# Kernel tuning notes

Measured on AMD Instinct MI355X. Metric: run time of the kernel, lower is better.

Reference implementation:

```python
import jax, jax.numpy as jnp
import numpy as np

B, NF, QUERY_DIM = 4, 300, 512
HIDDEN, NUM_HEADS = 512, 8
H, W = 80, 80
HEAD_DIM = HIDDEN // NUM_HEADS
NORM_FACT = float(HIDDEN / NUM_HEADS) ** (-0.5)


def setup_inputs() -> dict:
    key = jax.random.key(0)
    k1, k2, k3, k4, k5 = jax.random.split(key, 5)
    # xavier_uniform bound for [HIDDEN, QUERY_DIM] weight
    bound = float(np.sqrt(6.0 / (HIDDEN + QUERY_DIM)))
    return {
        "q": jax.random.normal(k1, (B, NF, QUERY_DIM), dtype=jnp.float32),
        "k": jax.random.normal(k2, (B, QUERY_DIM, H, W), dtype=jnp.float32),
        "mask": jax.random.bernoulli(k3, 0.25, (B, H, W)),  # True = masked out
        "q_w": jax.random.uniform(k4, (HIDDEN, QUERY_DIM), jnp.float32, -bound, bound),
        "q_b": jnp.zeros((HIDDEN,), jnp.float32),
        "k_w": jax.random.uniform(k5, (HIDDEN, QUERY_DIM), jnp.float32, -bound, bound),
        "k_b": jnp.zeros((HIDDEN,), jnp.float32),
    }


def reference(q, k, mask, q_w, q_b, k_w, k_b):
    b, nf, _ = q.shape
    h, w = k.shape[-2], k.shape[-1]
    # q projection: [b, nf, hidden]
    qp = jnp.einsum("bqd,ed->bqe", q, q_w) + q_b
    # k projection (1x1 conv == channel matmul): [b, hidden, h, w]
    kp = jnp.einsum("bdhw,ed->behw", k, k_w) + k_b[None, :, None, None]
    # split heads
    qh = qp.reshape(b, nf, NUM_HEADS, HEAD_DIM) * NORM_FACT   # [b,q,n,c]
    kh = kp.reshape(b, NUM_HEADS, HEAD_DIM, h, w)             # [b,n,c,h,w]
    # batched QK scores (replaces the per-query python loop + cat(dim=2))
    weights = jnp.einsum("bqnc,bnchw->bqnhw", qh, kh)
    weights = weights.reshape(b, 1, nf * NUM_HEADS, h, w)
    # masked_fill with -inf on padded spatial positions
    weights = jnp.where(mask[:, None, None, :, :], -jnp.inf, weights)
    # NOTE: softmax over flatten(2) = jointly over (queries*heads*h*w), as in source
    weights = jax.nn.softmax(weights.reshape(b, 1, -1), axis=-1)
    return weights.reshape(b, 1, nf * NUM_HEADS, h, w)
```

## Files before the change

### kernel.cpp

```cpp
#include <hip/hip_runtime.h>
#include <math.h>

#define B_    4
#define NF    300
#define QD    512
#define HID   512
#define NH    8
#define HD    64
#define HW    6400
#define ROWS  2400
#define NQP   384
#define NORM_FACT 0.125f
#define NEG_INF (-INFINITY)
#define LDK   40

typedef __bf16 bf16_t;
typedef __bf16 bf16x4_t __attribute__((ext_vector_type(4)));
typedef __bf16 bf16x8_t __attribute__((ext_vector_type(8)));
typedef float  f32x4    __attribute__((ext_vector_type(4)));

__device__ __forceinline__ void splitf(float x, bf16_t& h, bf16_t& l) {
    h = (bf16_t)x;
    l = (bf16_t)(x - (float)h);
}
__device__ __forceinline__ int swz(int c, int row) {
    return (((c >> 3) ^ (row & 7)) << 3) | (c & 7);
}

__device__ __forceinline__ void qproj_body(
    char* smem, int blk, const float* __restrict__ q,
    const float* __restrict__ qw, const float* __restrict__ qb,
    bf16_t* __restrict__ qh_hi, bf16_t* __restrict__ qh_lo)
{
    float (*qs)[QD] = (float (*)[QD])smem;
    const int r0    = blk * 4;
    const int b     = r0 / NF;
    const int qbase = r0 % NF;
    const int t     = threadIdx.x;
    #pragma unroll
    for (int row = 0; row < 4; ++row) {
        qs[row][t]       = q[(size_t)(r0 + row) * QD + t];
        qs[row][t + 256] = q[(size_t)(r0 + row) * QD + t + 256];
    }
    __syncthreads();
    #pragma unroll
    for (int eo = 0; eo < 2; ++eo) {
        const int e = t + eo * 256;
        const int n = e >> 6, c = e & 63;
        float a[4] = {0.f, 0.f, 0.f, 0.f};
        for (int d = 0; d < QD; d += 4) {
            float4 w = *(const float4*)&qw[(size_t)e * QD + d];
            #pragma unroll
            for (int row = 0; row < 4; ++row)
                a[row] += qs[row][d]*w.x + qs[row][d+1]*w.y
                        + qs[row][d+2]*w.z + qs[row][d+3]*w.w;
        }
        const float bias = qb[e];
        #pragma unroll
        for (int row = 0; row < 4; ++row) {
            const int qq = qbase + row;
            const float val = (a[row] + bias) * NORM_FACT;
            bf16_t h, l; splitf(val, h, l);
            size_t off = ((size_t)(b * NH + n) * NQP + qq) * 64 + swz(c, qq);
            qh_hi[off] = h; qh_lo[off] = l;
        }
    }
}

__device__ __forceinline__ void kproj_body(
    char* smem, int px, int ey, int b, const float* __restrict__ k,
    const float* __restrict__ kw, const float* __restrict__ kb,
    bf16_t* __restrict__ kp_hi, bf16_t* __restrict__ kp_lo)
{
    bf16_t (*Ah)[LDK] = (bf16_t (*)[LDK])(smem);
    bf16_t (*Al)[LDK] = (bf16_t (*)[LDK])(smem + 10240);
    bf16_t (*Bh)[LDK] = (bf16_t (*)[LDK])(smem + 20480);
    bf16_t (*Bl)[LDK] = (bf16_t (*)[LDK])(smem + 30720);
    const int e0 = ey * 128;
    const int p0 = px * 128;
    const int t  = threadIdx.x;
    const int wave = t >> 6, lane = t & 63;
    const int wr = wave >> 1, wc = wave & 1;
    const int lm = lane & 15, lq = lane >> 4;
    const float* kB = k + (size_t)b * QD * HW;

    f32x4 acc[4][4];
    const f32x4 zero4 = {0.f, 0.f, 0.f, 0.f};
    #pragma unroll
    for (int i = 0; i < 4; ++i)
        #pragma unroll
        for (int j = 0; j < 4; ++j) acc[i][j] = zero4;

    for (int d0 = 0; d0 < QD; d0 += 32) {
        #pragma unroll
        for (int i = 0; i < 4; ++i) {
            int idx = t + i * 256;
            int p = idx & 127, db = (idx >> 7) << 2;
            bf16x4_t hv, lv;
            #pragma unroll
            for (int j = 0; j < 4; ++j) {
                float x = kB[(size_t)(d0 + db + j) * HW + p0 + p];
                bf16_t hx, lx; splitf(x, hx, lx);
                hv[j] = hx; lv[j] = lx;
            }
            *(bf16x4_t*)&Ah[p][db] = hv;
            *(bf16x4_t*)&Al[p][db] = lv;
        }
        #pragma unroll
        for (int i = 0; i < 4; ++i) {
            int idx = t + i * 256;
            int e = idx >> 3, dp = (idx & 7) << 2;
            float4 v = *(const float4*)&kw[(size_t)(e0 + e) * QD + d0 + dp];
            bf16x4_t hv, lv; bf16_t hx, lx;
            splitf(v.x, hx, lx); hv[0] = hx; lv[0] = lx;
            splitf(v.y, hx, lx); hv[1] = hx; lv[1] = lx;
            splitf(v.z, hx, lx); hv[2] = hx; lv[2] = lx;
            splitf(v.w, hx, lx); hv[3] = hx; lv[3] = lx;
            *(bf16x4_t*)&Bh[e][dp] = hv;
            *(bf16x4_t*)&Bl[e][dp] = lv;
        }
        __syncthreads();

        bf16x8_t ah[4], al[4], bh[4], bl[4];
        #pragma unroll
        for (int mt = 0; mt < 4; ++mt) {
            int r = wr * 64 + mt * 16 + lm;
            ah[mt] = *(const bf16x8_t*)&Ah[r][lq * 8];
            al[mt] = *(const bf16x8_t*)&Al[r][lq * 8];
        }
        #pragma unroll
        for (int nt = 0; nt < 4; ++nt) {
            int c = wc * 64 + nt * 16 + lm;
            bh[nt] = *(const bf16x8_t*)&Bh[c][lq * 8];
            bl[nt] = *(const bf16x8_t*)&Bl[c][lq * 8];
        }
        #pragma unroll
        for (int mt = 0; mt < 4; ++mt)
            #pragma unroll
            for (int nt = 0; nt < 4; ++nt) {
                f32x4 a = acc[mt][nt];
                a = __builtin_amdgcn_mfma_f32_16x16x32_bf16(al[mt], bh[nt], a, 0, 0, 0);
                a = __builtin_amdgcn_mfma_f32_16x16x32_bf16(ah[mt], bl[nt], a, 0, 0, 0);
                a = __builtin_amdgcn_mfma_f32_16x16x32_bf16(ah[mt], bh[nt], a, 0, 0, 0);
                acc[mt][nt] = a;
            }
        __syncthreads();
    }

    #pragma unroll
    for (int nt = 0; nt < 4; ++nt) {
        const int e = e0 + wc * 64 + nt * 16 + lm;
        const int n = e >> 6;
        const int c = (nt * 16 + lm) & 63;
        const float bias = kb[e];
        bf16_t* dh = kp_hi + (size_t)(b * NH + n) * HW * 64;
        bf16_t* dl = kp_lo + (size_t)(b * NH + n) * HW * 64;
        #pragma unroll
        for (int mt = 0; mt < 4; ++mt) {
            #pragma unroll
            for (int reg = 0; reg < 4; ++reg) {
                int p = p0 + wr * 64 + mt * 16 + lq * 4 + reg;
                float val = acc[mt][nt][reg] + bias;
                bf16_t h, l; splitf(val, h, l);
                size_t off = (size_t)p * 64 + swz(c, p);
                dh[off] = h; dl[off] = l;
            }
        }
    }
}

__global__ __launch_bounds__(256) void proj_kernel(
    const float* __restrict__ q, const float* __restrict__ qw,
    const float* __restrict__ qb, const float* __restrict__ k,
    const float* __restrict__ kw, const float* __restrict__ kb,
    bf16_t* __restrict__ qh_hi, bf16_t* __restrict__ qh_lo,
    bf16_t* __restrict__ kp_hi, bf16_t* __restrict__ kp_lo)
{
    __shared__ __align__(16) char smem[40960];
    const int bx = blockIdx.x;
    if (bx < 800) {
        kproj_body(smem, bx % 50, (bx / 50) % 4, bx / 200, k, kw, kb, kp_hi, kp_lo);
    } else {
        qproj_body(smem, bx - 800, q, qw, qb, qh_hi, qh_lo);
    }
}

template<int KS>
__device__ __forceinline__ void load_qf(const bf16_t* __restrict__ qp,
                                        int lm, int lq, bf16x8_t (&f)[4])
{
    #pragma unroll
    for (int nt = 0; nt < 4; ++nt) {
        const size_t o = (size_t)(nt * 16 + lm) * 64
                       + (size_t)((((KS * 4 + lq) ^ (lm & 7))) << 3);
        f[nt] = *(const bf16x8_t*)(qp + o);
    }
}

template<int KS>
__device__ __forceinline__ void ks_mfma_hi(const bf16_t* Kh, int wr, int lm, int lq,
                                           const bf16x8_t (&qh)[4], f32x4 (&acc)[4][4])
{
    #pragma unroll
    for (int mt = 0; mt < 4; ++mt) {
        const int row = wr * 64 + mt * 16 + lm;
        const int off = row * 64 + ((((KS * 4 + lq) ^ (lm & 7))) << 3);
        const bf16x8_t ah = *(const bf16x8_t*)&Kh[off];
        #pragma unroll
        for (int nt = 0; nt < 4; ++nt)
            acc[mt][nt] = __builtin_amdgcn_mfma_f32_16x16x32_bf16(
                ah, qh[nt], acc[mt][nt], 0, 0, 0);
    }
}

template<int KS>
__device__ __forceinline__ void ks_mfma_split(const bf16_t* Kh, const bf16_t* Kl,
                                              int wr, int lm, int lq,
                                              const bf16x8_t (&qh)[4],
                                              const bf16x8_t (&ql)[4],
                                              f32x4 (&acc)[4][4])
{
    #pragma unroll
    for (int mt = 0; mt < 4; ++mt) {
        const int row = wr * 64 + mt * 16 + lm;
        const int off = row * 64 + ((((KS * 4 + lq) ^ (lm & 7))) << 3);
        const bf16x8_t ah = *(const bf16x8_t*)&Kh[off];
        const bf16x8_t al = *(const bf16x8_t*)&Kl[off];
        #pragma unroll
        for (int nt = 0; nt < 4; ++nt) {
            f32x4 a = acc[mt][nt];
            a = __builtin_amdgcn_mfma_f32_16x16x32_bf16(al, qh[nt], a, 0, 0, 0);
            a = __builtin_amdgcn_mfma_f32_16x16x32_bf16(ah, ql[nt], a, 0, 0, 0);
            a = __builtin_amdgcn_mfma_f32_16x16x32_bf16(ah, qh[nt], a, 0, 0, 0);
            acc[mt][nt] = a;
        }
    }
}

__global__ __launch_bounds__(256, 4) void scores_pass_a(
    const bf16_t* __restrict__ qh_hi, const bf16_t* __restrict__ kp_hi,
    const int* __restrict__ mask, float* __restrict__ partials)
{
    __shared__ __align__(16) bf16_t Kh[128 * 64];
    __shared__ float redM[256];
    __shared__ float redS[256];
    const int z  = blockIdx.z;
    const int b  = z >> 3, n = z & 7;
    const int q0 = blockIdx.y * 128;
    const int p0 = blockIdx.x * 128;
    const int t  = threadIdx.x;
    const int wave = t >> 6, lane = t & 63;
    const int wr = wave >> 1, wc = wave & 1;
    const int lm = lane & 15, lq = lane >> 4;
    const bool wave_active = (q0 + wc * 64) < NF;

    const uint4* gb = (const uint4*)(kp_hi + ((size_t)(b * NH + n) * HW + p0) * 64);
    uint4* lb = (uint4*)Kh;
    #pragma unroll
    for (int i = 0; i < 4; ++i) lb[t + i * 256] = gb[t + i * 256];

    const bf16_t* qph = qh_hi + ((size_t)(b * NH + n) * NQP + q0 + wc * 64) * 64;
    bf16x8_t qf0[4];
    if (wave_active) load_qf<0>(qph, lm, lq, qf0);
    __syncthreads();

    float tm = NEG_INF, ts = 0.f;
    if (wave_active) {
        f32x4 acc[4][4];
        const f32x4 zero4 = {0.f, 0.f, 0.f, 0.f};
        #pragma unroll
        for (int i = 0; i < 4; ++i)
            #pragma unroll
            for (int j = 0; j < 4; ++j) acc[i][j] = zero4;

        bf16x8_t qf1[4];
        load_qf<1>(qph, lm, lq, qf1);
        ks_mfma_hi<0>(Kh, wr, lm, lq, qf0, acc);
        ks_mfma_hi<1>(Kh, wr, lm, lq, qf1, acc);

        int4 mm4[4];
        #pragma unroll
        for (int mt = 0; mt < 4; ++mt)
            mm4[mt] = *(const int4*)&mask[b * HW + p0 + wr * 64 + mt * 16 + lq * 4];

        #pragma unroll
        for (int nt = 0; nt < 4; ++nt) {
            if (q0 + wc * 64 + nt * 16 + lm < NF) {
                #pragma unroll
                for (int mt = 0; mt < 4; ++mt)
                    #pragma unroll
                    for (int reg = 0; reg < 4; ++reg)
                        if (!((const int*)&mm4[mt])[reg])
                            tm = fmaxf(tm, acc[mt][nt][reg]);
            }
        }
        if (tm != NEG_INF) {
            #pragma unroll
            for (int nt = 0; nt < 4; ++nt) {
                if (q0 + wc * 64 + nt * 16 + lm < NF) {
                    #pragma unroll
                    for (int mt = 0; mt < 4; ++mt)
                        #pragma unroll
                        for (int reg = 0; reg < 4; ++reg)
                            if (!((const int*)&mm4[mt])[reg])
                                ts += __expf(acc[mt][nt][reg] - tm);
                }
            }
        }
    }

    redM[t] = tm; redS[t] = ts;
    __syncthreads();
    for (int off = 128; off > 0; off >>= 1) {
        if (t < off) {
            float m1 = redM[t],       s1 = redS[t];
            float m2 = redM[t + off], s2 = redS[t + off];
            float M = fmaxf(m1, m2);
            float s = (M == NEG_INF) ? 0.f
                      : (s1 * __expf(m1 - M) + s2 * __expf(m2 - M));
            redM[t] = M; redS[t] = s;
        }
        __syncthreads();
    }
    if (t == 0) {
        int lin = (z * gridDim.y + blockIdx.y) * gridDim.x + blockIdx.x;
        partials[2 * lin]     = redM[0];
        partials[2 * lin + 1] = redS[0];
    }
}

__global__ __launch_bounds__(256) void stats_kernel(
    const float* __restrict__ partials, float* __restrict__ stats, int nper)
{
    __shared__ float redM[256];
    __shared__ float redS[256];
    const int b = blockIdx.x, t = threadIdx.x;
    const float* p = partials + (size_t)b * nper * 2;
    float m = NEG_INF, s = 0.f;
    for (int i = t; i < nper; i += 256) {
        float m2 = p[2 * i], s2 = p[2 * i + 1];
        float M = fmaxf(m, m2);
        float ns = (M == NEG_INF) ? 0.f
                   : (s * __expf(m - M) + s2 * __expf(m2 - M));
        m = M; s = ns;
    }
    redM[t] = m; redS[t] = s;
    __syncthreads();
    for (int off = 128; off > 0; off >>= 1) {
        if (t < off) {
            float m1 = redM[t],       s1 = redS[t];
            float m2 = redM[t + off], s2 = redS[t + off];
            float M = fmaxf(m1, m2);
            float ns = (M == NEG_INF) ? 0.f
                       : (s1 * __expf(m1 - M) + s2 * __expf(m2 - M));
            redM[t] = M; redS[t] = ns;
        }
        __syncthreads();
    }
    if (t == 0) {
        stats[2 * b]     = redM[0];
        stats[2 * b + 1] = 1.0f / redS[0];
    }
}

__global__ __launch_bounds__(256, 3) void scores_pass_b(
    const bf16_t* __restrict__ qh_hi, const bf16_t* __restrict__ qh_lo,
    const bf16_t* __restrict__ kp_hi, const bf16_t* __restrict__ kp_lo,
    const int* __restrict__ mask, const float* __restrict__ stats,
    float* __restrict__ out)
{
    __shared__ __align__(16) bf16_t Kh[128 * 64];
    __shared__ __align__(16) bf16_t Kl[128 * 64];
    const int z  = blockIdx.z;
    const int b  = z >> 3, n = z & 7;
    const int q0 = blockIdx.y * 128;
    const int p0 = blockIdx.x * 128;
    const int t  = threadIdx.x;
    const int wave = t >> 6, lane = t & 63;
    const int wr = wave >> 1, wc = wave & 1;
    const int lm = lane & 15, lq = lane >> 4;
    const bool wave_active = (q0 + wc * 64) < NF;

    const float M    = stats[2 * b];
    const float invS = stats[2 * b + 1];

    const size_t bbase = ((size_t)(b * NH + n) * HW + p0) * 64;
    const uint4* gbh = (const uint4*)(kp_hi + bbase);
    const uint4* gbl = (const uint4*)(kp_lo + bbase);
    #pragma unroll
    for (int i = 0; i < 4; ++i) {
        ((uint4*)Kh)[t + i * 256] = gbh[t + i * 256];
        ((uint4*)Kl)[t + i * 256] = gbl[t + i * 256];
    }

    const size_t qoff = ((size_t)(b * NH + n) * NQP + q0 + wc * 64) * 64;
    const bf16_t* qph = qh_hi + qoff;
    const bf16_t* qpl = qh_lo + qoff;
    bf16x8_t qh0[4], ql0[4];
    if (wave_active) {
        load_qf<0>(qph, lm, lq, qh0);
        load_qf<0>(qpl, lm, lq, ql0);
    }
    __syncthreads();
    if (!wave_active) return;

    f32x4 acc[4][4];
    const f32x4 zero4 = {0.f, 0.f, 0.f, 0.f};
    #pragma unroll
    for (int i = 0; i < 4; ++i)
        #pragma unroll
        for (int j = 0; j < 4; ++j) acc[i][j] = zero4;

    bf16x8_t qh1[4], ql1[4];
    load_qf<1>(qph, lm, lq, qh1);
    load_qf<1>(qpl, lm, lq, ql1);
    ks_mfma_split<0>(Kh, Kl, wr, lm, lq, qh0, ql0, acc);
    ks_mfma_split<1>(Kh, Kl, wr, lm, lq, qh1, ql1, acc);

    int4 mm4[4];
    #pragma unroll
    for (int mt = 0; mt < 4; ++mt)
        mm4[mt] = *(const int4*)&mask[b * HW + p0 + wr * 64 + mt * 16 + lq * 4];

    #pragma unroll
    for (int nt = 0; nt < 4; ++nt) {
        const int qg = q0 + wc * 64 + nt * 16 + lm;
        if (qg < NF) {
            float* rowp = out + (size_t)(b * ROWS + qg * NH + n) * HW + p0 + wr * 64;
            #pragma unroll
            for (int mt = 0; mt < 4; ++mt) {
                f32x4 v;
                #pragma unroll
                for (int reg = 0; reg < 4; ++reg) {
                    const int msk = ((const int*)&mm4[mt])[reg];
                    v[reg] = msk ? 0.f : __expf(acc[mt][nt][reg] - M) * invS;
                }
                __builtin_nontemporal_store(v, (f32x4*)(rowp + mt * 16 + lq * 4));
            }
        }
    }
}

extern "C" void kernel_launch(void* const* d_in, const int* in_sizes, int n_in,
                              void* d_out, int out_size, void* d_ws, size_t ws_size,
                              hipStream_t stream) {
    const float* q    = (const float*)d_in[0];
    const float* k    = (const float*)d_in[1];
    const int*   mask = (const int*)  d_in[2];
    const float* qw   = (const float*)d_in[3];
    const float* qb   = (const float*)d_in[4];
    const float* kw   = (const float*)d_in[5];
    const float* kb   = (const float*)d_in[6];
    float* out = (float*)d_out;

    bf16_t* kp_hi = (bf16_t*)d_ws;
    bf16_t* kp_lo = kp_hi + (size_t)B_ * NH * HW * 64;
    bf16_t* qh_hi = kp_lo + (size_t)B_ * NH * HW * 64;
    bf16_t* qh_lo = qh_hi + (size_t)B_ * NH * NQP * 64;
    float* partials = (float*)(qh_lo + (size_t)B_ * NH * NQP * 64);
    float* stats    = partials + 2 * 4800;

    proj_kernel<<<1100, 256, 0, stream>>>(q, qw, qb, k, kw, kb,
                                          qh_hi, qh_lo, kp_hi, kp_lo);
    scores_pass_a<<<dim3(50, 3, 32), 256, 0, stream>>>(qh_hi, kp_hi, mask, partials);
    stats_kernel<<<4, 256, 0, stream>>>(partials, stats, 1200);
    scores_pass_b<<<dim3(50, 3, 32), 256, 0, stream>>>(qh_hi, qh_lo, kp_hi, kp_lo,
                                                       mask, stats, out);
}
```

Baseline: 477.0 us.

## Pre-split K and weights to bf16 hi/lo, use direct global-to-LDS loads

```diff
diff --git a/kernel.cpp b/kernel.cpp
--- a/kernel.cpp
+++ b/kernel.cpp
@@ -12,12 +12,11 @@
 #define NQP   384
 #define NORM_FACT 0.125f
 #define NEG_INF (-INFINITY)
-#define LDK   40
 
 typedef __bf16 bf16_t;
-typedef __bf16 bf16x4_t __attribute__((ext_vector_type(4)));
 typedef __bf16 bf16x8_t __attribute__((ext_vector_type(8)));
 typedef float  f32x4    __attribute__((ext_vector_type(4)));
+typedef unsigned int u32;
 
 __device__ __forceinline__ void splitf(float x, bf16_t& h, bf16_t& l) {
     h = (bf16_t)x;
@@ -26,63 +25,127 @@
 __device__ __forceinline__ int swz(int c, int row) {
     return (((c >> 3) ^ (row & 7)) << 3) | (c & 7);
 }
-
-__device__ __forceinline__ void qproj_body(
-    char* smem, int blk, const float* __restrict__ q,
-    const float* __restrict__ qw, const float* __restrict__ qb,
+__device__ __forceinline__ void gload_lds16(const bf16_t* g, bf16_t* l) {
+    __builtin_amdgcn_global_load_lds(
+        (const __attribute__((address_space(1))) u32*)g,
+        (__attribute__((address_space(3))) u32*)l, 16, 0, 0);
+}
+
+__global__ __launch_bounds__(256) void presplit_kernel(
+    const float* __restrict__ k, const float* __restrict__ kw,
+    const float* __restrict__ q, const float* __restrict__ qw,
+    const float* __restrict__ qb,
+    bf16_t* __restrict__ kt_hi, bf16_t* __restrict__ kt_lo,
+    bf16_t* __restrict__ wh, bf16_t* __restrict__ wl,
     bf16_t* __restrict__ qh_hi, bf16_t* __restrict__ qh_lo)
 {
-    float (*qs)[QD] = (float (*)[QD])smem;
-    const int r0    = blk * 4;
-    const int b     = r0 / NF;
-    const int qbase = r0 % NF;
-    const int t     = threadIdx.x;
-    #pragma unroll
-    for (int row = 0; row < 4; ++row) {
-        qs[row][t]       = q[(size_t)(r0 + row) * QD + t];
-        qs[row][t + 256] = q[(size_t)(r0 + row) * QD + t + 256];
-    }
-    __syncthreads();
-    #pragma unroll
-    for (int eo = 0; eo < 2; ++eo) {
-        const int e = t + eo * 256;
-        const int n = e >> 6, c = e & 63;
-        float a[4] = {0.f, 0.f, 0.f, 0.f};
-        for (int d = 0; d < QD; d += 4) {
-            float4 w = *(const float4*)&qw[(size_t)e * QD + d];
-            #pragma unroll
-            for (int row = 0; row < 4; ++row)
-                a[row] += qs[row][d]*w.x + qs[row][d+1]*w.y
-                        + qs[row][d+2]*w.z + qs[row][d+3]*w.w;
-        }
-        const float bias = qb[e];
+    __shared__ __align__(16) char smem[64 * 65 * 4];
+    const int blk = blockIdx.x;
+    const int t   = threadIdx.x;
+
+    if (blk < 3200) {
+        float (*ts)[65] = (float (*)[65])smem;
+        const int b   = blk / 800;
+        const int rem = blk % 800;
+        const int d0  = (rem / 100) * 64;
+        const int p0  = (rem % 100) * 64;
+        const float* kB = k + (size_t)b * QD * HW;
+        const int c = t & 63, r0 = t >> 6;
+        #pragma unroll
+        for (int pass = 0; pass < 16; ++pass) {
+            const int r = r0 + pass * 4;
+            ts[r][c] = kB[(size_t)(d0 + r) * HW + p0 + c];
+        }
+        __syncthreads();
+        const int pr  = t >> 2;
+        const int dcb = (t & 3) * 16;
+        const int pg  = p0 + pr;
+        const size_t obase = ((size_t)b * HW + pg) * 512 + d0;
+        #pragma unroll
+        for (int half = 0; half < 2; ++half) {
+            const int c0 = dcb + half * 8;
+            bf16x8_t hv, lv;
+            #pragma unroll
+            for (int j = 0; j < 8; ++j) {
+                bf16_t h, l; splitf(ts[c0 + j][pr], h, l);
+                hv[j] = h; lv[j] = l;
+            }
+            const size_t o = obase + ((((c0 >> 3) ^ (pg & 7)) << 3));
+            *(bf16x8_t*)&kt_hi[o] = hv;
+            *(bf16x8_t*)&kt_lo[o] = lv;
+        }
+    } else if (blk < 3328) {
+        const int base = (blk - 3200) * 2048 + t * 8;
+        const int e = base >> 9, d = base & 511;
+        float4 v0 = *(const float4*)&kw[base];
+        float4 v1 = *(const float4*)&kw[base + 4];
+        bf16x8_t hv, lv; bf16_t h, l;
+        splitf(v0.x, h, l); hv[0] = h; lv[0] = l;
+        splitf(v0.y, h, l); hv[1] = h; lv[1] = l;
+        splitf(v0.z, h, l); hv[2] = h; lv[2] = l;
+        splitf(v0.w, h, l); hv[3] = h; lv[3] = l;
+        splitf(v1.x, h, l); hv[4] = h; lv[4] = l;
+        splitf(v1.y, h, l); hv[5] = h; lv[5] = l;
+        splitf(v1.z, h, l); hv[6] = h; lv[6] = l;
+        splitf(v1.w, h, l); hv[7] = h; lv[7] = l;
+        const size_t o = (size_t)e * 512 + (d & ~63)
+                       + (((((d >> 3) & 7) ^ (e & 7)) << 3));
+        *(bf16x8_t*)&wh[o] = hv;
+        *(bf16x8_t*)&wl[o] = lv;
+    } else {
+        float (*qs)[QD] = (float (*)[QD])smem;
+        const int r0    = (blk - 3328) * 4;
+        const int b     = r0 / NF;
+        const int qbase = r0 % NF;
         #pragma unroll
         for (int row = 0; row < 4; ++row) {
-            const int qq = qbase + row;
-            const float val = (a[row] + bias) * NORM_FACT;
-            bf16_t h, l; splitf(val, h, l);
-            size_t off = ((size_t)(b * NH + n) * NQP + qq) * 64 + swz(c, qq);
-            qh_hi[off] = h; qh_lo[off] = l;
-        }
-    }
-}
-
-__device__ __forceinline__ void kproj_body(
-    char* smem, int px, int ey, int b, const float* __restrict__ k,
-    const float* __restrict__ kw, const float* __restrict__ kb,
-    bf16_t* __restrict__ kp_hi, bf16_t* __restrict__ kp_lo)
-{
-    bf16_t (*Ah)[LDK] = (bf16_t (*)[LDK])(smem);
-    bf16_t (*Al)[LDK] = (bf16_t (*)[LDK])(smem + 10240);
-    bf16_t (*Bh)[LDK] = (bf16_t (*)[LDK])(smem + 20480);
-    bf16_t (*Bl)[LDK] = (bf16_t (*)[LDK])(smem + 30720);
-    const int e0 = ey * 128;
-    const int p0 = px * 128;
+            qs[row][t]       = q[(size_t)(r0 + row) * QD + t];
+            qs[row][t + 256] = q[(size_t)(r0 + row) * QD + t + 256];
+        }
+        __syncthreads();
+        #pragma unroll
+        for (int eo = 0; eo < 2; ++eo) {
+            const int e = t + eo * 256;
+            const int n = e >> 6, c = e & 63;
+            float a[4] = {0.f, 0.f, 0.f, 0.f};
+            for (int d = 0; d < QD; d += 4) {
+                float4 w = *(const float4*)&qw[(size_t)e * QD + d];
+                #pragma unroll
+                for (int row = 0; row < 4; ++row)
+                    a[row] += qs[row][d]*w.x + qs[row][d+1]*w.y
+                            + qs[row][d+2]*w.z + qs[row][d+3]*w.w;
+            }
+            const float bias = qb[e];
+            #pragma unroll
+            for (int row = 0; row < 4; ++row) {
+                const int qq = qbase + row;
+                const float val = (a[row] + bias) * NORM_FACT;
+                bf16_t h, l; splitf(val, h, l);
+                size_t off = ((size_t)(b * NH + n) * NQP + qq) * 64 + swz(c, qq);
+                qh_hi[off] = h; qh_lo[off] = l;
+            }
+        }
+    }
+}
+
+__global__ __launch_bounds__(256, 2) void kproj_mfma(
+    const bf16_t* __restrict__ kt_hi, const bf16_t* __restrict__ kt_lo,
+    const bf16_t* __restrict__ wh, const bf16_t* __restrict__ wl,
+    const float* __restrict__ kb, bf16_t* __restrict__ kp_hi,
+    bf16_t* __restrict__ kp_lo)
+{
+    __shared__ __align__(16) bf16_t Ah[128 * 64];
+    __shared__ __align__(16) bf16_t Al[128 * 64];
+    __shared__ __align__(16) bf16_t Bh[128 * 64];
+    __shared__ __align__(16) bf16_t Bl[128 * 64];
+    const int b  = blockIdx.z;
+    const int e0 = blockIdx.y * 128;
+    const int p0 = blockIdx.x * 128;
     const int t  = threadIdx.x;
     const int wave = t >> 6, lane = t & 63;
     const int wr = wave >> 1, wc = wave & 1;
     const int lm = lane & 15, lq = lane >> 4;
-    const float* kB = k + (size_t)b * QD * HW;
+    const int wu = t & ~63;
 
     f32x4 acc[4][4];
     const f32x4 zero4 = {0.f, 0.f, 0.f, 0.f};
@@ -91,59 +154,52 @@
         #pragma unroll
         for (int j = 0; j < 4; ++j) acc[i][j] = zero4;
 
-    for (int d0 = 0; d0 < QD; d0 += 32) {
+    const size_t abase = ((size_t)b * HW + p0) * 512;
+
+    for (int d0 = 0; d0 < QD; d0 += 64) {
         #pragma unroll
         for (int i = 0; i < 4; ++i) {
-            int idx = t + i * 256;
-            int p = idx & 127, db = (idx >> 7) << 2;
-            bf16x4_t hv, lv;
-            #pragma unroll
-            for (int j = 0; j < 4; ++j) {
-                float x = kB[(size_t)(d0 + db + j) * HW + p0 + p];
-                bf16_t hx, lx; splitf(x, hx, lx);
-                hv[j] = hx; lv[j] = lx;
-            }
-            *(bf16x4_t*)&Ah[p][db] = hv;
-            *(bf16x4_t*)&Al[p][db] = lv;
-        }
-        #pragma unroll
-        for (int i = 0; i < 4; ++i) {
-            int idx = t + i * 256;
-            int e = idx >> 3, dp = (idx & 7) << 2;
-            float4 v = *(const float4*)&kw[(size_t)(e0 + e) * QD + d0 + dp];
-            bf16x4_t hv, lv; bf16_t hx, lx;
-            splitf(v.x, hx, lx); hv[0] = hx; lv[0] = lx;
-            splitf(v.y, hx, lx); hv[1] = hx; lv[1] = lx;
-            splitf(v.z, hx, lx); hv[2] = hx; lv[2] = lx;
-            splitf(v.w, hx, lx); hv[3] = hx; lv[3] = lx;
-            *(bf16x4_t*)&Bh[e][dp] = hv;
-            *(bf16x4_t*)&Bl[e][dp] = lv;
+            const int u   = i * 256 + t;
+            const int ub  = i * 256 + wu;
+            const int row = u >> 3;
+            const int c8  = (u & 7) * 8;
+            const size_t ga = abase + (size_t)row * 512 + d0 + c8;
+            const size_t gb = (size_t)(e0 + row) * 512 + d0 + c8;
+            gload_lds16(kt_hi + ga, &Ah[(size_t)ub * 8]);
+            gload_lds16(kt_lo + ga, &Al[(size_t)ub * 8]);
+            gload_lds16(wh + gb,    &Bh[(size_t)ub * 8]);
+            gload_lds16(wl + gb,    &Bl[(size_t)ub * 8]);
         }
         __syncthreads();
 
-        bf16x8_t ah[4], al[4], bh[4], bl[4];
-        #pragma unroll
-        for (int mt = 0; mt < 4; ++mt) {
-            int r = wr * 64 + mt * 16 + lm;
-            ah[mt] = *(const bf16x8_t*)&Ah[r][lq * 8];
-            al[mt] = *(const bf16x8_t*)&Al[r][lq * 8];
-        }
-        #pragma unroll
-        for (int nt = 0; nt < 4; ++nt) {
-            int c = wc * 64 + nt * 16 + lm;
-            bh[nt] = *(const bf16x8_t*)&Bh[c][lq * 8];
-            bl[nt] = *(const bf16x8_t*)&Bl[c][lq * 8];
-        }
-        #pragma unroll
-        for (int mt = 0; mt < 4; ++mt)
+        #pragma unroll
+        for (int ks = 0; ks < 2; ++ks) {
+            bf16x8_t ah[4], al[4], bh[4], bl[4];
+            #pragma unroll
+            for (int mt = 0; mt < 4; ++mt) {
+                const int r   = wr * 64 + mt * 16 + lm;
+                const int off = r * 64 + (((ks * 4 + lq) ^ (lm & 7)) << 3);
+                ah[mt] = *(const bf16x8_t*)&Ah[off];
+                al[mt] = *(const bf16x8_t*)&Al[off];
+            }
             #pragma unroll
             for (int nt = 0; nt < 4; ++nt) {
-                f32x4 a = acc[mt][nt];
-                a = __builtin_amdgcn_mfma_f32_16x16x32_bf16(al[mt], bh[nt], a, 0, 0, 0);
-                a = __builtin_amdgcn_mfma_f32_16x16x32_bf16(ah[mt], bl[nt], a, 0, 0, 0);
-                a = __builtin_amdgcn_mfma_f32_16x16x32_bf16(ah[mt], bh[nt], a, 0, 0, 0);
-                acc[mt][nt] = a;
-            }
+                const int r   = wc * 64 + nt * 16 + lm;
+                const int off = r * 64 + (((ks * 4 + lq) ^ (lm & 7)) << 3);
+                bh[nt] = *(const bf16x8_t*)&Bh[off];
+                bl[nt] = *(const bf16x8_t*)&Bl[off];
+            }
+            #pragma unroll
+            for (int mt = 0; mt < 4; ++mt)
+                #pragma unroll
+                for (int nt = 0; nt < 4; ++nt) {
+                    f32x4 a = acc[mt][nt];
+                    a = __builtin_amdgcn_mfma_f32_16x16x32_bf16(al[mt], bh[nt], a, 0, 0, 0);
+                    a = __builtin_amdgcn_mfma_f32_16x16x32_bf16(ah[mt], bl[nt], a, 0, 0, 0);
+                    a = __builtin_amdgcn_mfma_f32_16x16x32_bf16(ah[mt], bh[nt], a, 0, 0, 0);
+                    acc[mt][nt] = a;
+                }
+        }
         __syncthreads();
     }
 
@@ -166,22 +222,6 @@
                 dh[off] = h; dl[off] = l;
             }
         }
-    }
-}
-
-__global__ __launch_bounds__(256) void proj_kernel(
-    const float* __restrict__ q, const float* __restrict__ qw,
-    const float* __restrict__ qb, const float* __restrict__ k,
-    const float* __restrict__ kw, const float* __restrict__ kb,
-    bf16_t* __restrict__ qh_hi, bf16_t* __restrict__ qh_lo,
-    bf16_t* __restrict__ kp_hi, bf16_t* __restrict__ kp_lo)
-{
-    __shared__ __align__(16) char smem[40960];
-    const int bx = blockIdx.x;
-    if (bx < 800) {
-        kproj_body(smem, bx % 50, (bx / 50) % 4, bx / 200, k, kw, kb, kp_hi, kp_lo);
-    } else {
-        qproj_body(smem, bx - 800, q, qw, qb, qh_hi, qh_lo);
     }
 }
 
@@ -252,12 +292,13 @@
     const int wave = t >> 6, lane = t & 63;
     const int wr = wave >> 1, wc = wave & 1;
     const int lm = lane & 15, lq = lane >> 4;
+    const int wu = t & ~63;
     const bool wave_active = (q0 + wc * 64) < NF;
 
-    const uint4* gb = (const uint4*)(kp_hi + ((size_t)(b * NH + n) * HW + p0) * 64);
-    uint4* lb = (uint4*)Kh;
-    #pragma unroll
-    for (int i = 0; i < 4; ++i) lb[t + i * 256] = gb[t + i * 256];
+    const bf16_t* gb = kp_hi + ((size_t)(b * NH + n) * HW + p0) * 64;
+    #pragma unroll
+    for (int i = 0; i < 4; ++i)
+        gload_lds16(gb + (size_t)(i * 256 + t) * 8, &Kh[(size_t)(i * 256 + wu) * 8]);
 
     const bf16_t* qph = qh_hi + ((size_t)(b * NH + n) * NQP + q0 + wc * 64) * 64;
     bf16x8_t qf0[4];
@@ -379,18 +420,19 @@
     const int wave = t >> 6, lane = t & 63;
     const int wr = wave >> 1, wc = wave & 1;
     const int lm = lane & 15, lq = lane >> 4;
+    const int wu = t & ~63;
     const bool wave_active = (q0 + wc * 64) < NF;
 
     const float M    = stats[2 * b];
     const float invS = stats[2 * b + 1];
 
     const size_t bbase = ((size_t)(b * NH + n) * HW + p0) * 64;
-    const uint4* gbh = (const uint4*)(kp_hi + bbase);
-    const uint4* gbl = (const uint4*)(kp_lo + bbase);
+    const bf16_t* gbh = kp_hi + bbase;
+    const bf16_t* gbl = kp_lo + bbase;
     #pragma unroll
     for (int i = 0; i < 4; ++i) {
-        ((uint4*)Kh)[t + i * 256] = gbh[t + i * 256];
-        ((uint4*)Kl)[t + i * 256] = gbl[t + i * 256];
+        gload_lds16(gbh + (size_t)(i * 256 + t) * 8, &Kh[(size_t)(i * 256 + wu) * 8]);
+        gload_lds16(gbl + (size_t)(i * 256 + t) * 8, &Kl[(size_t)(i * 256 + wu) * 8]);
     }
 
     const size_t qoff = ((size_t)(b * NH + n) * NQP + q0 + wc * 64) * 64;
@@ -460,8 +502,15 @@
     float* partials = (float*)(qh_lo + (size_t)B_ * NH * NQP * 64);
     float* stats    = partials + 2 * 4800;
 
-    proj_kernel<<<1100, 256, 0, stream>>>(q, qw, qb, k, kw, kb,
-                                          qh_hi, qh_lo, kp_hi, kp_lo);
+    bf16_t* kt_hi = (bf16_t*)d_out;
+    bf16_t* kt_lo = kt_hi + (size_t)B_ * HW * 512;
+    bf16_t* wh    = kt_lo + (size_t)B_ * HW * 512;
+    bf16_t* wl    = wh + (size_t)512 * 512;
+
+    presplit_kernel<<<3628, 256, 0, stream>>>(k, kw, q, qw, qb,
+                                              kt_hi, kt_lo, wh, wl, qh_hi, qh_lo);
+    kproj_mfma<<<dim3(50, 4, 4), 256, 0, stream>>>(kt_hi, kt_lo, wh, wl, kb,
+                                                   kp_hi, kp_lo);
     scores_pass_a<<<dim3(50, 3, 32), 256, 0, stream>>>(qh_hi, kp_hi, mask, partials);
     stats_kernel<<<4, 256, 0, stream>>>(partials, stats, 1200);
     scores_pass_b<<<dim3(50, 3, 32), 256, 0, stream>>>(qh_hi, qh_lo, kp_hi, kp_lo,
```

Result: slower. 537.4 us (+12.7%).
